# Performance work log

Hardware: AMD Instinct MI355X
Metric: run time of the kernel (lower is better)

Reference implementation:

```python
import jax, jax.numpy as jnp
import numpy as np
from jax import lax

# ---- static graph layout: GPT-2-small-like full edge-pruning config ----
N_LAYERS, H = 12, 12
V_TOTAL = 2 + N_LAYERS * (H + 1)  # wte, wpe, then per layer: H attn outputs + 1 mlp

def _layer_dims(L):
    Vq = 2 + L * (H + 1)  # vertices visible to q/k/v at layer L (strictly upstream)
    Vm = Vq + H           # mlp additionally sees same-layer attn outputs
    return Vq, Vm

_LAYER_BASE = []
_p = 0
for _L in range(N_LAYERS):
    _LAYER_BASE.append(_p)
    _Vq, _Vm = _layer_dims(_L)
    _p += 3 * H * _Vq + _Vm  # q,k,v edges for all heads, then mlp edges
_LM_BASE = _p
P_TOTAL = _p + V_TOTAL       # lm_head reads every vertex


def _keep(Rch):
    """Given per-vertex reachability Rch (bz, V_TOTAL) bool, build the per-edge
    keep mask (bz, P_TOTAL): an edge survives iff its output vertex AND its
    input vertex are both reachable (== ~dangling in the torch code)."""
    bz = Rch.shape[0]
    parts = []
    for L in range(N_LAYERS):
        Vq, Vm = _layer_dims(L)
        a0 = 2 + L * (H + 1)
        ar = Rch[:, a0:a0 + H]        # (bz, H) attn_output-L-h reach
        mr = Rch[:, a0 + H]           # (bz,)  mlp-L reach
        kq = ar[:, None, :, None] & Rch[:, None, None, :Vq]  # (bz,3,H,Vq)
        parts.append(jnp.broadcast_to(kq, (bz, 3, H, Vq)).reshape(bz, 3 * H * Vq))
        parts.append(mr[:, None] & Rch[:, :Vm])
        del kq
    parts.append(Rch)                 # lm_head edges: keep iff input reachable
    return jnp.concatenate(parts, axis=1)


def _prune_dangling_edges(masks):
    bz = masks.shape[0]
    # --- forward reachability (reach-to-input), no-grad boolean sweep ---
    pos = masks > 0.0
    R = jnp.ones((bz, 2), bool)  # wte, wpe always reachable
    for L in range(N_LAYERS):
        Vq, Vm = _layer_dims(L)
        b = _LAYER_BASE[L]
        qkv = pos[:, b:b + 3 * H * Vq].reshape(bz, 3, H, Vq)
        # head reachable iff q AND k AND v each have >=1 live reachable input
        ar = jnp.all(jnp.any(qkv & R[:, None, None, :], axis=-1), axis=1)  # (bz,H)
        R = jnp.concatenate([R, ar], axis=1)                               # size Vm
        mm = pos[:, b + 3 * H * Vq: b + 3 * H * Vq + Vm]
        mr = jnp.any(mm & R, axis=-1)
        R = jnp.concatenate([R, mr[:, None]], axis=1)
    masks = jnp.where(_keep(R), masks, 0.0)
    # --- backward reachability (reach-to-output) on the pruned masks ---
    pos = masks > 0.0
    O = pos[:, _LM_BASE:]  # (bz, V_TOTAL): vertices fed into lm_head
    for L in range(N_LAYERS - 1, -1, -1):
        Vq, Vm = _layer_dims(L)
        b = _LAYER_BASE[L]
        a0 = 2 + L * (H + 1)
        # mlp first (it may make same-layer attn outputs output-reachable)
        mm = pos[:, b + 3 * H * Vq: b + 3 * H * Vq + Vm]
        O = O.at[:, :Vm].set(O[:, :Vm] | (mm & O[:, a0 + H][:, None]))
        qkv = pos[:, b:b + 3 * H * Vq].reshape(bz, 3, H, Vq)
        contrib = jnp.any(qkv & O[:, None, a0:a0 + H, None], axis=(1, 2))  # (bz,Vq)
        O = O.at[:, :Vq].set(O[:, :Vq] | contrib)
    masks = jnp.where(_keep(O), masks, 0.0)
    return masks


def setup_inputs() -> dict:
    key = jax.random.key(0)
    k1, k2 = jax.random.split(key)
    bz = 1024
    sample_params = jax.random.normal(k1, (P_TOTAL,), dtype=jnp.float32)
    unif = jax.random.uniform(k2, (bz, P_TOTAL), dtype=jnp.float32)
    return {"sample_params": sample_params, "unif": unif}


def reference(sample_params, unif):
    bz = unif.shape[0]
    prob = jnp.broadcast_to(jax.nn.sigmoid(sample_params)[None, :], unif.shape)
    window = lax.stop_gradient(prob * (1.0 - prob))  # detached window size
    prob = window * prob + (1.0 - window) * lax.stop_gradient(prob)
    masks = jnp.clip((prob - unif) / window + 0.5, 0.0, 1.0)
    masks = _prune_dangling_edges(masks)
    active = (masks > 0.001) & (masks < 1.0 - 0.001)
    n_samples = jnp.sum(active, axis=0).astype(masks.dtype)  # (P,)
    grad_wts = lax.stop_gradient(
        jnp.where(n_samples < 1.0, 0.0, bz / jnp.maximum(n_samples, 1.0)))
    masks = grad_wts * masks + (1.0 - grad_wts) * lax.stop_gradient(masks)
    return masks
```

## Files before the change

kernel.cpp:

```cpp
#include <hip/hip_runtime.h>
#include <stdint.h>

#define NL   12
#define PTOT 32936
#define LMB  32778
#define NCH  515
#define NCHP 520
#define NGRP 129
#define BMW  (NGRP * 4)
#define TPAD (NGRP * 256)
#define NSEG 445
#define TPB  512
#define NWV  (TPB / 64)
#define NITER ((NGRP + NWV - 1) / NWV)

typedef float vf4 __attribute__((ext_vector_type(4)));

__device__ __constant__ int c_base[NL] = {0,86,653,1701,3230,5240,7731,10703,14156,18090,22505,27401};

__device__ __forceinline__ uint64_t ext(const uint64_t* P, uint32_t off) {
  uint32_t w = off >> 6, s = off & 63;
  uint64_t lo = P[w], hi = P[w + 1];
  return s ? ((lo >> s) | (hi << (64 - s))) : lo;
}

__device__ __forceinline__ uint64_t rbit(uint64_t r0, uint64_t r1, uint64_t r2, uint32_t idx) {
  uint64_t w = idx < 64 ? r0 : (idx < 128 ? r1 : r2);
  return (w >> (idx & 63)) & 1ull;
}

__device__ __forceinline__ uint64_t rext(uint64_t a0, uint64_t a1, uint64_t a2, uint32_t off) {
  uint32_t w = off >> 6, s = off & 63;
  uint64_t lo = (w == 0) ? a0 : ((w == 1) ? a1 : ((w == 2) ? a2 : 0ull));
  uint64_t hi = (w == 0) ? a1 : ((w == 1) ? a2 : 0ull);
  return s ? ((lo >> s) | (hi << (64 - s))) : lo;
}

__device__ __forceinline__ void orAt(uint64_t& r0, uint64_t& r1, uint64_t& r2,
                                     uint64_t val, uint32_t pos) {
  uint32_t w = pos >> 6, s = pos & 63;
  uint64_t lo = val << s;
  uint64_t hi = s ? (val >> (64 - s)) : 0ull;
  if (w == 0) { r0 |= lo; r1 |= hi; }
  else if (w == 1) { r1 |= lo; r2 |= hi; }
  else { r2 |= lo; }
}

__device__ __forceinline__ void maskLen(uint32_t len, uint64_t& m0, uint64_t& m1, uint64_t& m2) {
  m0 = (len >= 64) ? ~0ull : ((1ull << len) - 1ull);
  m1 = (len <= 64) ? 0ull : ((len >= 128) ? ~0ull : ((1ull << (len - 64)) - 1ull));
  m2 = (len <= 128) ? 0ull : ((1ull << (len - 128)) - 1ull);
}

__device__ __forceinline__ uint32_t ext12(uint64_t O0, uint64_t O1, uint64_t O2, uint32_t pos) {
  uint32_t w = pos >> 6, s = pos & 63;
  uint64_t lo = (w == 0) ? O0 : ((w == 1) ? O1 : O2);
  uint64_t hi = (w == 0) ? O1 : ((w == 1) ? O2 : 0ull);
  uint64_t v = s ? ((lo >> s) | (hi << (64 - s))) : lo;
  return (uint32_t)v & 0xFFFu;
}

__device__ __forceinline__ uint64_t spread4(uint64_t x) {
  x = (x | (x << 24)) & 0x000000FF000000FFull;
  x = (x | (x << 12)) & 0x000F000F000F000Full;
  x = (x | (x << 6))  & 0x0303030303030303ull;
  x = (x | (x << 3))  & 0x1111111111111111ull;
  return x;
}

__global__ void init_tables(const float* __restrict__ sp, float* __restrict__ pr,
                            float* __restrict__ wd) {
  int p = blockIdx.x * blockDim.x + threadIdx.x;
  if (p >= TPAD) return;
  if (p < PTOT) {
    float x = sp[p];
    float s = 1.0f / (1.0f + expf(-x));
    float w = __fmul_rn(s, __fsub_rn(1.0f, s));
    float pv = __fadd_rn(__fmul_rn(w, s), __fmul_rn(__fsub_rn(1.0f, w), s));
    pr[p] = pv; wd[p] = w;
  } else {
    pr[p] = 0.0f; wd[p] = 1.0f;
  }
}

__global__ __launch_bounds__(TPB, 3) void fused_kernel(const float* __restrict__ unif,
                                                       const vf4* __restrict__ pr4,
                                                       const vf4* __restrict__ wd4,
                                                       float* __restrict__ out) {
  __shared__ uint64_t sPos[NCHP];
  __shared__ uint64_t sKeep[NCHP];
  __shared__ uint64_t sLv[4];

  const int tid  = threadIdx.x;
  const int lane = tid & 63;
  const int wv   = tid >> 6;
  const int row  = blockIdx.x;
  const vf4* up4 = (const vf4*)(unif + (size_t)row * PTOT);
  vf4*       op4 = (vf4*)(out + (size_t)row * PTOT);

  vf4 mv[NITER];
  vf4 ub[4], pb[2], wb[2];

#define LDU(K) do { int G_ = wv + (K) * NWV; if (G_ < NGRP) {                  \
    int e4_ = G_ * 64 + lane;                                                  \
    ub[(K) % 4] = (e4_ < (PTOT / 4)) ? up4[e4_] : (vf4){0.f,0.f,0.f,0.f}; } } while (0)
#define LDPW(K) do { int G_ = wv + (K) * NWV; if (G_ < NGRP) {                 \
    int e4_ = G_ * 64 + lane;                                                  \
    pb[(K) % 2] = pr4[e4_]; wb[(K) % 2] = wd4[e4_]; } } while (0)

  LDU(0); LDU(1); LDU(2); LDU(3); LDPW(0); LDPW(1);
  for (int w = tid; w < NCHP; w += TPB) sKeep[w] = 0ull;
  for (int w = BMW + tid; w < NCHP; w += TPB) sPos[w] = 0ull;

#pragma unroll
  for (int k = 0; k < NITER; ++k) {
    const int G = wv + k * NWV;
    if (G < NGRP) {
      vf4 u = ub[k % 4], p = pb[k % 2], w = wb[k % 2];
      int e4 = G * 64 + lane;
      bool inb = e4 < (PTOT / 4);
      float m0 = __fadd_rn(__fdiv_rn(__fsub_rn(p.x, u.x), w.x), 0.5f);
      float m1 = __fadd_rn(__fdiv_rn(__fsub_rn(p.y, u.y), w.y), 0.5f);
      float m2 = __fadd_rn(__fdiv_rn(__fsub_rn(p.z, u.z), w.z), 0.5f);
      float m3 = __fadd_rn(__fdiv_rn(__fsub_rn(p.w, u.w), w.w), 0.5f);
      mv[k] = (vf4){fminf(fmaxf(m0, 0.0f), 1.0f), fminf(fmaxf(m1, 0.0f), 1.0f),
                    fminf(fmaxf(m2, 0.0f), 1.0f), fminf(fmaxf(m3, 0.0f), 1.0f)};
      uint64_t b0 = __ballot(inb && (m0 > 0.0f));
      uint64_t b1 = __ballot(inb && (m1 > 0.0f));
      uint64_t b2 = __ballot(inb && (m2 > 0.0f));
      uint64_t b3 = __ballot(inb && (m3 > 0.0f));
      if (lane < 4) {
        int q = lane;
        uint64_t v = spread4((b0 >> (16 * q)) & 0xFFFFull)
                   | (spread4((b1 >> (16 * q)) & 0xFFFFull) << 1)
                   | (spread4((b2 >> (16 * q)) & 0xFFFFull) << 2)
                   | (spread4((b3 >> (16 * q)) & 0xFFFFull) << 3);
        sPos[4 * G + q] = v;
      }
    }
    if (k + 4 < NITER) LDU(k + 4);
    if (k + 2 < NITER) LDPW(k + 2);
  }
#undef LDU
#undef LDPW
  __syncthreads();

  if (tid < 64) {
    uint64_t R0 = 3ull, R1 = 0ull, R2 = 0ull;
    const int g = lane;
#pragma unroll
    for (int L = 0; L < NL; ++L) {
      const int Vq = 2 + 13 * L;
      const int b  = c_base[L];
      bool pred = false;
      if (g < 36) {
        uint32_t off = (uint32_t)(b + g * Vq);
        uint64_t e0 = ext(sPos, off), e1 = ext(sPos, off + 64), e2 = ext(sPos, off + 128);
        pred = ((e0 & R0) | (e1 & R1) | (e2 & R2)) != 0ull;
      }
      uint64_t bal = __ballot(pred);
      uint64_t ar  = bal & (bal >> 12) & (bal >> 24) & 0xFFFull;
      orAt(R0, R1, R2, ar, (uint32_t)Vq);
      const int Vm = Vq + 12;
      uint32_t offm = (uint32_t)(b + 36 * Vq);
      uint64_t e0 = ext(sPos, offm), e1 = ext(sPos, offm + 64), e2 = ext(sPos, offm + 128);
      uint64_t mr = (((e0 & R0) | (e1 & R1) | (e2 & R2)) != 0ull) ? 1ull : 0ull;
      orAt(R0, R1, R2, mr, (uint32_t)Vm);
    }

    uint64_t O0 = ext(sPos, LMB)       & R0;
    uint64_t O1 = ext(sPos, LMB + 64)  & R1;
    uint64_t O2 = ext(sPos, LMB + 128) & ((1ull << 30) - 1ull) & R2;
    const int hg = g % 12;
#pragma unroll
    for (int L = NL - 1; L >= 0; --L) {
      const int Vq = 2 + 13 * L, Vm = Vq + 12;
      const int b  = c_base[L];
      if (rbit(O0, O1, O2, (uint32_t)Vm)) {
        uint64_t m0, m1, m2; maskLen((uint32_t)Vm, m0, m1, m2);
        uint32_t offm = (uint32_t)(b + 36 * Vq);
        O0 |= ext(sPos, offm)       & R0 & m0;
        O1 |= ext(sPos, offm + 64)  & R1 & m1;
        O2 |= ext(sPos, offm + 128) & R2 & m2;
      }
      uint32_t h12 = ext12(O0, O1, O2, (uint32_t)Vq);
      uint64_t q0, q1, q2; maskLen((uint32_t)Vq, q0, q1, q2);
      uint64_t c0 = 0ull, c1 = 0ull, c2 = 0ull;
      if (g < 36 && ((h12 >> hg) & 1u)) {
        uint32_t off = (uint32_t)(b + g * Vq);
        c0 = ext(sPos, off)       & R0 & q0;
        c1 = ext(sPos, off + 64)  & R1 & q1;
        c2 = ext(sPos, off + 128) & R2 & q2;
      }
#pragma unroll
      for (int d = 32; d; d >>= 1) {
        c0 |= __shfl_xor((unsigned long long)c0, d);
        c1 |= __shfl_xor((unsigned long long)c1, d);
        c2 |= __shfl_xor((unsigned long long)c2, d);
      }
      O0 |= c0; O1 |= c1; O2 |= c2;
    }
    if (lane == 0) {
      sLv[0] = R0 & O0; sLv[1] = R1 & O1; sLv[2] = R2 & O2; sLv[3] = 0ull;
    }
  }
  __syncthreads();

  {
    const uint64_t l0 = sLv[0], l1 = sLv[1], l2 = sLv[2];
    for (int s = tid; s < NSEG; s += TPB) {
      uint32_t p0, len;
      bool olive;
      if (s == NSEG - 1) {
        p0 = LMB; len = 158; olive = true;
      } else {
        int L = s / 37, j = s - L * 37;
        int Vq = 2 + 13 * L, b = c_base[L];
        if (j < 36) { p0 = (uint32_t)(b + j * Vq); len = (uint32_t)Vq;
                      olive = rbit(l0, l1, l2, (uint32_t)(Vq + (j % 12))) != 0ull; }
        else        { p0 = (uint32_t)(b + 36 * Vq); len = (uint32_t)(Vq + 12);
                      olive = rbit(l0, l1, l2, (uint32_t)(Vq + 12)) != 0ull; }
      }
      if (!olive) continue;
      uint32_t w0 = p0 >> 6, s0 = p0 & 63;
      uint64_t first = l0;
      if (len < 64) first &= (1ull << len) - 1ull;
      atomicOr((unsigned long long*)&sKeep[w0], (unsigned long long)(first << s0));
      uint32_t done = 64 - s0;
      uint32_t w = w0 + 1;
      while (done < len) {
        uint64_t v = rext(l0, l1, l2, done);
        uint32_t rem = len - done;
        if (rem < 64) v &= (1ull << rem) - 1ull;
        atomicOr((unsigned long long*)&sKeep[w], (unsigned long long)v);
        done += 64; ++w;
      }
    }
  }
  __syncthreads();

  {
    const int sh = 4 * (lane & 15);
    const int kw0 = lane >> 4;
#pragma unroll
    for (int k = 0; k < NITER; ++k) {
      const int G = wv + k * NWV;
      if (G >= NGRP) continue;
      int e4 = G * 64 + lane;
      bool inb = e4 < (PTOT / 4);
      uint32_t kb = (uint32_t)(sKeep[G * 4 + kw0] >> sh) & 0xFu;
      vf4 m = mv[k];
      if (inb) {
        vf4 o;
        o.x = (kb & 1u) ? m.x : 0.0f;
        o.y = (kb & 2u) ? m.y : 0.0f;
        o.z = (kb & 4u) ? m.z : 0.0f;
        o.w = (kb & 8u) ? m.w : 0.0f;
        __builtin_nontemporal_store(o, &op4[e4]);
      }
    }
  }
}

extern "C" void kernel_launch(void* const* d_in, const int* in_sizes, int n_in,
                              void* d_out, int out_size, void* d_ws, size_t ws_size,
                              hipStream_t stream) {
  const float* sp   = (const float*)d_in[0];
  const float* unif = (const float*)d_in[1];
  float* out = (float*)d_out;
  char* ws = (char*)d_ws;
  float* pr = (float*)ws;
  float* wd = (float*)(ws + 132096);
  int bz = in_sizes[1] / PTOT;

  init_tables<<<dim3(TPAD / 256), dim3(256), 0, stream>>>(sp, pr, wd);
  fused_kernel<<<dim3(bz), dim3(TPB), 0, stream>>>(
      unif, (const vf4*)pr, (const vf4*)wd, out);
}
```

Before: 255.1 us.

## Process two rows per block, overlapping second row's loads with first's graph pass

Each block now handles two batch rows. The second row's uniform loads are issued before the first row's serial graph-reachability phase, and the second row's mask compute is fused into the first row's store loop. This hides latency behind the single-wave reachability sweep. Launch bounds are raised to 4 blocks per SM while the grid is halved. In exchange there is more register pressure from holding both rows' data, an assumption that the batch size is even, and a wave count of 512 blocks, which may underfill the GPU.

```diff
diff --git a/kernel.cpp b/kernel.cpp
--- a/kernel.cpp
+++ b/kernel.cpp
@@ -68,6 +68,97 @@
   return x;
 }
 
+__device__ __forceinline__ void graph_live(const uint64_t* sPos, uint64_t* sLv, int lane) {
+  uint64_t R0 = 3ull, R1 = 0ull, R2 = 0ull;
+  const int g = lane;
+#pragma unroll
+  for (int L = 0; L < NL; ++L) {
+    const int Vq = 2 + 13 * L;
+    const int b  = c_base[L];
+    bool pred = false;
+    if (g < 36) {
+      uint32_t off = (uint32_t)(b + g * Vq);
+      uint64_t e0 = ext(sPos, off), e1 = ext(sPos, off + 64), e2 = ext(sPos, off + 128);
+      pred = ((e0 & R0) | (e1 & R1) | (e2 & R2)) != 0ull;
+    }
+    uint64_t bal = __ballot(pred);
+    uint64_t ar  = bal & (bal >> 12) & (bal >> 24) & 0xFFFull;
+    orAt(R0, R1, R2, ar, (uint32_t)Vq);
+    const int Vm = Vq + 12;
+    uint32_t offm = (uint32_t)(b + 36 * Vq);
+    uint64_t e0 = ext(sPos, offm), e1 = ext(sPos, offm + 64), e2 = ext(sPos, offm + 128);
+    uint64_t mr = (((e0 & R0) | (e1 & R1) | (e2 & R2)) != 0ull) ? 1ull : 0ull;
+    orAt(R0, R1, R2, mr, (uint32_t)Vm);
+  }
+  uint64_t O0 = ext(sPos, LMB)       & R0;
+  uint64_t O1 = ext(sPos, LMB + 64)  & R1;
+  uint64_t O2 = ext(sPos, LMB + 128) & ((1ull << 30) - 1ull) & R2;
+  const int hg = g % 12;
+#pragma unroll
+  for (int L = NL - 1; L >= 0; --L) {
+    const int Vq = 2 + 13 * L, Vm = Vq + 12;
+    const int b  = c_base[L];
+    if (rbit(O0, O1, O2, (uint32_t)Vm)) {
+      uint64_t m0, m1, m2; maskLen((uint32_t)Vm, m0, m1, m2);
+      uint32_t offm = (uint32_t)(b + 36 * Vq);
+      O0 |= ext(sPos, offm)       & R0 & m0;
+      O1 |= ext(sPos, offm + 64)  & R1 & m1;
+      O2 |= ext(sPos, offm + 128) & R2 & m2;
+    }
+    uint32_t h12 = ext12(O0, O1, O2, (uint32_t)Vq);
+    uint64_t q0, q1, q2; maskLen((uint32_t)Vq, q0, q1, q2);
+    uint64_t c0 = 0ull, c1 = 0ull, c2 = 0ull;
+    if (g < 36 && ((h12 >> hg) & 1u)) {
+      uint32_t off = (uint32_t)(b + g * Vq);
+      c0 = ext(sPos, off)       & R0 & q0;
+      c1 = ext(sPos, off + 64)  & R1 & q1;
+      c2 = ext(sPos, off + 128) & R2 & q2;
+    }
+#pragma unroll
+    for (int d = 32; d; d >>= 1) {
+      c0 |= __shfl_xor((unsigned long long)c0, d);
+      c1 |= __shfl_xor((unsigned long long)c1, d);
+      c2 |= __shfl_xor((unsigned long long)c2, d);
+    }
+    O0 |= c0; O1 |= c1; O2 |= c2;
+  }
+  if (lane == 0) {
+    sLv[0] = R0 & O0; sLv[1] = R1 & O1; sLv[2] = R2 & O2; sLv[3] = 0ull;
+  }
+}
+
+__device__ __forceinline__ void build_keep(uint64_t* sKeep, const uint64_t* sLv, int tid) {
+  const uint64_t l0 = sLv[0], l1 = sLv[1], l2 = sLv[2];
+  for (int s = tid; s < NSEG; s += TPB) {
+    uint32_t p0, len;
+    bool olive;
+    if (s == NSEG - 1) {
+      p0 = LMB; len = 158; olive = true;
+    } else {
+      int L = s / 37, j = s - L * 37;
+      int Vq = 2 + 13 * L, b = c_base[L];
+      if (j < 36) { p0 = (uint32_t)(b + j * Vq); len = (uint32_t)Vq;
+                    olive = rbit(l0, l1, l2, (uint32_t)(Vq + (j % 12))) != 0ull; }
+      else        { p0 = (uint32_t)(b + 36 * Vq); len = (uint32_t)(Vq + 12);
+                    olive = rbit(l0, l1, l2, (uint32_t)(Vq + 12)) != 0ull; }
+    }
+    if (!olive) continue;
+    uint32_t w0 = p0 >> 6, s0 = p0 & 63;
+    uint64_t first = l0;
+    if (len < 64) first &= (1ull << len) - 1ull;
+    atomicOr((unsigned long long*)&sKeep[w0], (unsigned long long)(first << s0));
+    uint32_t done = 64 - s0;
+    uint32_t w = w0 + 1;
+    while (done < len) {
+      uint64_t v = rext(l0, l1, l2, done);
+      uint32_t rem = len - done;
+      if (rem < 64) v &= (1ull << rem) - 1ull;
+      atomicOr((unsigned long long*)&sKeep[w], (unsigned long long)v);
+      done += 64; ++w;
+    }
+  }
+}
+
 __global__ void init_tables(const float* __restrict__ sp, float* __restrict__ pr,
                             float* __restrict__ wd) {
   int p = blockIdx.x * blockDim.x + threadIdx.x;
@@ -83,7 +174,7 @@
   }
 }
 
-__global__ __launch_bounds__(TPB, 3) void fused_kernel(const float* __restrict__ unif,
+__global__ __launch_bounds__(TPB, 4) void fused_kernel(const float* __restrict__ unif,
                                                        const vf4* __restrict__ pr4,
                                                        const vf4* __restrict__ wd4,
                                                        float* __restrict__ out) {
@@ -94,21 +185,23 @@
   const int tid  = threadIdx.x;
   const int lane = tid & 63;
   const int wv   = tid >> 6;
-  const int row  = blockIdx.x;
-  const vf4* up4 = (const vf4*)(unif + (size_t)row * PTOT);
-  vf4*       op4 = (vf4*)(out + (size_t)row * PTOT);
+  const int row0 = blockIdx.x * 2;
+  const vf4* up0 = (const vf4*)(unif + (size_t)row0 * PTOT);
+  const vf4* up1 = (const vf4*)(unif + (size_t)(row0 + 1) * PTOT);
+  vf4*       op0 = (vf4*)(out + (size_t)row0 * PTOT);
+  vf4*       op1 = (vf4*)(out + (size_t)(row0 + 1) * PTOT);
 
   vf4 mv[NITER];
   vf4 ub[4], pb[2], wb[2];
 
-#define LDU(K) do { int G_ = wv + (K) * NWV; if (G_ < NGRP) {                  \
+#define LDU(PTR, K) do { int G_ = wv + (K) * NWV; if (G_ < NGRP) {             \
     int e4_ = G_ * 64 + lane;                                                  \
-    ub[(K) % 4] = (e4_ < (PTOT / 4)) ? up4[e4_] : (vf4){0.f,0.f,0.f,0.f}; } } while (0)
+    ub[(K) % 4] = (e4_ < (PTOT / 4)) ? (PTR)[e4_] : (vf4){0.f,0.f,0.f,0.f}; } } while (0)
 #define LDPW(K) do { int G_ = wv + (K) * NWV; if (G_ < NGRP) {                 \
     int e4_ = G_ * 64 + lane;                                                  \
     pb[(K) % 2] = pr4[e4_]; wb[(K) % 2] = wd4[e4_]; } } while (0)
 
-  LDU(0); LDU(1); LDU(2); LDU(3); LDPW(0); LDPW(1);
+  LDU(up0, 0); LDU(up0, 1); LDU(up0, 2); LDU(up0, 3); LDPW(0); LDPW(1);
   for (int w = tid; w < NCHP; w += TPB) sKeep[w] = 0ull;
   for (int w = BMW + tid; w < NCHP; w += TPB) sPos[w] = 0ull;
 
@@ -138,105 +231,73 @@
         sPos[4 * G + q] = v;
       }
     }
-    if (k + 4 < NITER) LDU(k + 4);
+    if (k + 4 < NITER) LDU(up0, k + 4);
     if (k + 2 < NITER) LDPW(k + 2);
+  }
+  LDU(up1, 0); LDU(up1, 1); LDU(up1, 2); LDU(up1, 3); LDPW(0); LDPW(1);
+  __syncthreads();
+
+  if (tid < 64) graph_live(sPos, sLv, lane);
+  __syncthreads();
+
+  build_keep(sKeep, sLv, tid);
+  __syncthreads();
+
+  {
+    const int sh = 4 * (lane & 15);
+    const int kw0 = lane >> 4;
+#pragma unroll
+    for (int k = 0; k < NITER; ++k) {
+      const int G = wv + k * NWV;
+      if (G < NGRP) {
+        int e4 = G * 64 + lane;
+        bool inb = e4 < (PTOT / 4);
+        uint32_t kb = (uint32_t)(sKeep[G * 4 + kw0] >> sh) & 0xFu;
+        vf4 m = mv[k];
+        if (inb) {
+          vf4 o;
+          o.x = (kb & 1u) ? m.x : 0.0f;
+          o.y = (kb & 2u) ? m.y : 0.0f;
+          o.z = (kb & 4u) ? m.z : 0.0f;
+          o.w = (kb & 8u) ? m.w : 0.0f;
+          __builtin_nontemporal_store(o, &op0[e4]);
+        }
+        vf4 u = ub[k % 4], p = pb[k % 2], w = wb[k % 2];
+        float m0 = __fadd_rn(__fdiv_rn(__fsub_rn(p.x, u.x), w.x), 0.5f);
+        float m1 = __fadd_rn(__fdiv_rn(__fsub_rn(p.y, u.y), w.y), 0.5f);
+        float m2 = __fadd_rn(__fdiv_rn(__fsub_rn(p.z, u.z), w.z), 0.5f);
+        float m3 = __fadd_rn(__fdiv_rn(__fsub_rn(p.w, u.w), w.w), 0.5f);
+        mv[k] = (vf4){fminf(fmaxf(m0, 0.0f), 1.0f), fminf(fmaxf(m1, 0.0f), 1.0f),
+                      fminf(fmaxf(m2, 0.0f), 1.0f), fminf(fmaxf(m3, 0.0f), 1.0f)};
+        uint64_t b0 = __ballot(inb && (m0 > 0.0f));
+        uint64_t b1 = __ballot(inb && (m1 > 0.0f));
+        uint64_t b2 = __ballot(inb && (m2 > 0.0f));
+        uint64_t b3 = __ballot(inb && (m3 > 0.0f));
+        if (lane < 4) {
+          int q = lane;
+          uint64_t v = spread4((b0 >> (16 * q)) & 0xFFFFull)
+                     | (spread4((b1 >> (16 * q)) & 0xFFFFull) << 1)
+                     | (spread4((b2 >> (16 * q)) & 0xFFFFull) << 2)
+                     | (spread4((b3 >> (16 * q)) & 0xFFFFull) << 3);
+          sPos[4 * G + q] = v;
+        }
+      }
+      if (k + 4 < NITER) LDU(up1, k + 4);
+      if (k + 2 < NITER) LDPW(k + 2);
+    }
   }
 #undef LDU
 #undef LDPW
   __syncthreads();
 
   if (tid < 64) {
-    uint64_t R0 = 3ull, R1 = 0ull, R2 = 0ull;
-    const int g = lane;
-#pragma unroll
-    for (int L = 0; L < NL; ++L) {
-      const int Vq = 2 + 13 * L;
-      const int b  = c_base[L];
-      bool pred = false;
-      if (g < 36) {
-        uint32_t off = (uint32_t)(b + g * Vq);
-        uint64_t e0 = ext(sPos, off), e1 = ext(sPos, off + 64), e2 = ext(sPos, off + 128);
-        pred = ((e0 & R0) | (e1 & R1) | (e2 & R2)) != 0ull;
-      }
-      uint64_t bal = __ballot(pred);
-      uint64_t ar  = bal & (bal >> 12) & (bal >> 24) & 0xFFFull;
-      orAt(R0, R1, R2, ar, (uint32_t)Vq);
-      const int Vm = Vq + 12;
-      uint32_t offm = (uint32_t)(b + 36 * Vq);
-      uint64_t e0 = ext(sPos, offm), e1 = ext(sPos, offm + 64), e2 = ext(sPos, offm + 128);
-      uint64_t mr = (((e0 & R0) | (e1 & R1) | (e2 & R2)) != 0ull) ? 1ull : 0ull;
-      orAt(R0, R1, R2, mr, (uint32_t)Vm);
-    }
-
-    uint64_t O0 = ext(sPos, LMB)       & R0;
-    uint64_t O1 = ext(sPos, LMB + 64)  & R1;
-    uint64_t O2 = ext(sPos, LMB + 128) & ((1ull << 30) - 1ull) & R2;
-    const int hg = g % 12;
-#pragma unroll
-    for (int L = NL - 1; L >= 0; --L) {
-      const int Vq = 2 + 13 * L, Vm = Vq + 12;
-      const int b  = c_base[L];
-      if (rbit(O0, O1, O2, (uint32_t)Vm)) {
-        uint64_t m0, m1, m2; maskLen((uint32_t)Vm, m0, m1, m2);
-        uint32_t offm = (uint32_t)(b + 36 * Vq);
-        O0 |= ext(sPos, offm)       & R0 & m0;
-        O1 |= ext(sPos, offm + 64)  & R1 & m1;
-        O2 |= ext(sPos, offm + 128) & R2 & m2;
-      }
-      uint32_t h12 = ext12(O0, O1, O2, (uint32_t)Vq);
-      uint64_t q0, q1, q2; maskLen((uint32_t)Vq, q0, q1, q2);
-      uint64_t c0 = 0ull, c1 = 0ull, c2 = 0ull;
-      if (g < 36 && ((h12 >> hg) & 1u)) {
-        uint32_t off = (uint32_t)(b + g * Vq);
-        c0 = ext(sPos, off)       & R0 & q0;
-        c1 = ext(sPos, off + 64)  & R1 & q1;
-        c2 = ext(sPos, off + 128) & R2 & q2;
-      }
-#pragma unroll
-      for (int d = 32; d; d >>= 1) {
-        c0 |= __shfl_xor((unsigned long long)c0, d);
-        c1 |= __shfl_xor((unsigned long long)c1, d);
-        c2 |= __shfl_xor((unsigned long long)c2, d);
-      }
-      O0 |= c0; O1 |= c1; O2 |= c2;
-    }
-    if (lane == 0) {
-      sLv[0] = R0 & O0; sLv[1] = R1 & O1; sLv[2] = R2 & O2; sLv[3] = 0ull;
-    }
-  }
-  __syncthreads();
-
-  {
-    const uint64_t l0 = sLv[0], l1 = sLv[1], l2 = sLv[2];
-    for (int s = tid; s < NSEG; s += TPB) {
-      uint32_t p0, len;
-      bool olive;
-      if (s == NSEG - 1) {
-        p0 = LMB; len = 158; olive = true;
-      } else {
-        int L = s / 37, j = s - L * 37;
-        int Vq = 2 + 13 * L, b = c_base[L];
-        if (j < 36) { p0 = (uint32_t)(b + j * Vq); len = (uint32_t)Vq;
-                      olive = rbit(l0, l1, l2, (uint32_t)(Vq + (j % 12))) != 0ull; }
-        else        { p0 = (uint32_t)(b + 36 * Vq); len = (uint32_t)(Vq + 12);
-                      olive = rbit(l0, l1, l2, (uint32_t)(Vq + 12)) != 0ull; }
-      }
-      if (!olive) continue;
-      uint32_t w0 = p0 >> 6, s0 = p0 & 63;
-      uint64_t first = l0;
-      if (len < 64) first &= (1ull << len) - 1ull;
-      atomicOr((unsigned long long*)&sKeep[w0], (unsigned long long)(first << s0));
-      uint32_t done = 64 - s0;
-      uint32_t w = w0 + 1;
-      while (done < len) {
-        uint64_t v = rext(l0, l1, l2, done);
-        uint32_t rem = len - done;
-        if (rem < 64) v &= (1ull << rem) - 1ull;
-        atomicOr((unsigned long long*)&sKeep[w], (unsigned long long)v);
-        done += 64; ++w;
-      }
-    }
-  }
+    graph_live(sPos, sLv, lane);
+  } else {
+    for (int w = tid - 64; w < NCHP; w += TPB - 64) sKeep[w] = 0ull;
+  }
+  __syncthreads();
+
+  build_keep(sKeep, sLv, tid);
   __syncthreads();
 
   {
@@ -256,7 +317,7 @@
         o.y = (kb & 2u) ? m.y : 0.0f;
         o.z = (kb & 4u) ? m.z : 0.0f;
         o.w = (kb & 8u) ? m.w : 0.0f;
-        __builtin_nontemporal_store(o, &op4[e4]);
+        __builtin_nontemporal_store(o, &op1[e4]);
       }
     }
   }
@@ -274,6 +335,6 @@
   int bz = in_sizes[1] / PTOT;
 
   init_tables<<<dim3(TPAD / 256), dim3(256), 0, stream>>>(sp, pr, wd);
-  fused_kernel<<<dim3(bz), dim3(TPB), 0, stream>>>(
+  fused_kernel<<<dim3(bz / 2), dim3(TPB), 0, stream>>>(
       unif, (const vf4*)pr, (const vf4*)wd, out);
 }
```

Result: slower. 324.4 us (+27.2%).
